# Optimization experiments

Measured on AMD Instinct MI355X. Metric: run time of the kernel, lower is better.

## Reference

```python
import jax, jax.numpy as jnp
import numpy as np

L = 3          # num_layer
E_DIM = 64     # emb_dim
B = 4          # graphs per batch
N = 20000      # nodes per graph
E = 320000     # edges per graph
IN_DIM = 21    # raw node feature dim (Linear(21, emb_dim))
BN_EPS = 1e-5


def setup_inputs() -> dict:
    key = jax.random.key(0)
    ks = jax.random.split(key, 16)
    h2 = 2 * E_DIM
    inp = {
        "x": jax.random.normal(ks[0], (B, N, IN_DIM), dtype=jnp.float32),
        "edge_index": jax.random.randint(ks[1], (B, 2, E), 0, N, dtype=jnp.int64),
        "edge_attr": jax.random.normal(ks[2], (B, E, 1), dtype=jnp.float32),
        # layer-0 input node embedding Linear(21, emb)
        "inW": jax.random.normal(ks[3], (IN_DIM, E_DIM), dtype=jnp.float32) * 0.1,
        "inb": jnp.zeros((E_DIM,), dtype=jnp.float32),
        # per-layer edge encoder Linear(1, emb)
        "edgeW": jax.random.normal(ks[4], (L, 1, E_DIM), dtype=jnp.float32) * 0.1,
        "edgeb": jnp.zeros((L, E_DIM), dtype=jnp.float32),
        # per-layer MLP: Linear(2e,2e) -> BN(2e) -> ReLU -> Linear(2e,e)
        "W1": jax.random.normal(ks[5], (L, h2, h2), dtype=jnp.float32) * 0.05,
        "b1": jnp.zeros((L, h2), dtype=jnp.float32),
        "gamma": jnp.ones((L, h2), dtype=jnp.float32),
        "beta": jnp.zeros((L, h2), dtype=jnp.float32),
        "W2": jax.random.normal(ks[6], (L, h2, E_DIM), dtype=jnp.float32) * 0.05,
        "b2": jnp.zeros((L, E_DIM), dtype=jnp.float32),
    }
    return inp


def _batchnorm_train(h, g, b):
    # BatchNorm1d in training mode: per-graph stats over the node dim, biased var
    m = h.mean(axis=0)
    v = jnp.mean((h - m) ** 2, axis=0)
    return (h - m) * jax.lax.rsqrt(v + BN_EPS) * g + b


def _gin_layer(xg, eig, eag, W1l, b1l, gl, bel, W2l, b2l):
    # xg [N,e], eig [2,E], eag [E,e]
    x_j = xg[eig[0]]                                   # gather source nodes [E,e]
    msg = jnp.concatenate([x_j, eag], axis=-1)         # [E,2e]
    aggr = jax.ops.segment_sum(msg, eig[1], num_segments=N)  # scatter-add [N,2e]
    h = aggr @ W1l + b1l
    h = _batchnorm_train(h, gl, bel)
    h = jax.nn.relu(h)
    return h @ W2l + b2l                               # [N,e]


def reference(x, edge_index, edge_attr, inW, inb, edgeW, edgeb, W1, b1, gamma, beta, W2, b2):
    h = x
    for l in range(L):
        ea = edge_attr @ edgeW[l] + edgeb[l]           # [B,E,e] edge embeddings
        if l == 0:
            h = h @ inW + inb                          # [B,N,e]
        h = jax.vmap(_gin_layer, in_axes=(0, 0, 0, None, None, None, None, None, None))(
            h, edge_index, ea, W1[l], b1[l], gamma[l], beta[l], W2[l], b2[l])
        if l < L - 1:                                  # drop_ratio=0 -> dropout is identity
            h = jax.nn.relu(h)
    return h  # JK='last'
```

## Files before the change

kernel.cpp:

```cpp
#include <hip/hip_runtime.h>
#include <hip/hip_bf16.h>

#define NB 4
#define NN 20000
#define NE 320000
#define IND 21
#define ED 64
#define H2 128
#define CAP 48
#define RNODES 2500
#define ECHUNK 2560
#define BN_EPS 1e-5f

typedef __attribute__((ext_vector_type(8))) short bf16x8;
typedef __attribute__((ext_vector_type(4))) float f32x4;

__device__ __forceinline__ short f2bf(float f) {
    unsigned u = __float_as_uint(f);
    u += 0x7fffu + ((u >> 16) & 1u);
    return (short)(u >> 16);
}


__global__ __launch_bounds__(256) void k_fill_direct(
    const int* __restrict__ ei, const float* __restrict__ eattr,
    int* __restrict__ cnt, unsigned int* __restrict__ bucket)
{
    const int b = blockIdx.y;
    const int range = blockIdx.x & 7;
    const int chunk = blockIdx.x >> 3;
    const int lo = range * RNODES, hi = lo + RNODES;
    const int* srcp = ei + (size_t)b * 2 * NE;
    const int* dstp = srcp + NE;
    const float* ap = eattr + (size_t)b * NE;
    #pragma unroll
    for (int it = 0; it < ECHUNK / 256; ++it) {
        const int e = chunk * ECHUNK + it * 256 + threadIdx.x;
        const int dst = dstp[e];
        if (dst >= lo && dst < hi) {
            const int src = srcp[e];
            const float a = ap[e];
            const int node = b * NN + dst;
            const int p = atomicAdd(&cnt[node], 1);
            if (p < CAP)
                bucket[(size_t)node * CAP + p] =
                    ((unsigned int)src & 0xffffu) | (__float_as_uint(a) & 0xffff0000u);
        }
    }
}

__global__ __launch_bounds__(256) void k_sattr(
    const unsigned int* __restrict__ bucket, const int* __restrict__ cnt,
    float* __restrict__ s_attr)
{
    const int n = blockIdx.x * 256 + threadIdx.x;
    if (n >= NB * NN) return;
    const int c = min(cnt[n], CAP);
    const unsigned int* row = bucket + (size_t)n * CAP;
    float s = 0.f;
    for (int j = 0; j < c; ++j)
        s += __uint_as_float(row[j] & 0xffff0000u);
    s_attr[n] = s;
}

__global__ __launch_bounds__(256) void k_in(
    const float* __restrict__ x, const float* __restrict__ inW,
    const float* __restrict__ inb, float* __restrict__ h)
{
    const int b = blockIdx.y;
    const int t = blockIdx.x * 256 + threadIdx.x;
    const int n = t >> 6;
    const int c = t & 63;
    if (n >= NN) return;
    const float* xr = x + ((size_t)b * NN + n) * IND;
    float acc = inb[c];
    #pragma unroll
    for (int k = 0; k < IND; ++k) acc += xr[k] * inW[k * ED + c];
    h[((size_t)b * NN + n) * ED + c] = acc;
}

__global__ __launch_bounds__(256) void k_wconv(
    const float* __restrict__ W1, const float* __restrict__ W2,
    short* __restrict__ W1T, short* __restrict__ W2T)
{
    const int lyr = blockIdx.x;
    for (int i = threadIdx.x; i < H2 * ED; i += 256) {
        const int j = i >> 6, k = i & 63;
        W1T[lyr * 8192 + i] = f2bf(W1[(size_t)lyr * H2 * H2 + k * H2 + j]);
    }
    for (int i = threadIdx.x; i < ED * H2; i += 256) {
        const int c = i >> 7, k = i & 127;
        W2T[lyr * 8192 + i] = f2bf(W2[(size_t)lyr * H2 * ED + k * ED + c]);
    }
}


__global__ void k_uv_zero(const float* __restrict__ edgeW, const float* __restrict__ edgeb,
                          const float* __restrict__ W1, float* __restrict__ uv,
                          float* __restrict__ stats, int l)
{
    const int j = threadIdx.x;
    ((float4*)stats)[j] = make_float4(0.f, 0.f, 0.f, 0.f);
    if (j >= H2) return;
    float u = 0.f, v = 0.f;
    for (int k = 0; k < ED; ++k) {
        const float w = W1[(size_t)l * H2 * H2 + (ED + k) * H2 + j];
        u += edgeW[l * ED + k] * w;
        v += edgeb[l * ED + k] * w;
    }
    uv[j] = u;
    uv[H2 + j] = v;
}

__global__ __launch_bounds__(256) void k_aggr_stats(
    const float* __restrict__ h, const unsigned int* __restrict__ bucket,
    const int* __restrict__ cnt_arr, const float* __restrict__ s_attr,
    const short* __restrict__ W1Tl, const float* __restrict__ b1l,
    const float* __restrict__ uv, short* __restrict__ aggr_bf,
    float* __restrict__ stats)
{
    __shared__ short w1t[H2 * 72];
    __shared__ short atb[16 * 72];
    __shared__ float sdl[16], ddl[16];
    __shared__ float uL[H2], vL[H2], bbL[H2];
    const int tid = threadIdx.x;
    const int g = blockIdx.x & 7;
    const int b = g >> 1;
    const int t = ((int)blockIdx.x >> 3) * 2 + (g & 1);
    const int n0 = t * 16;

    for (int i = tid; i < 1024; i += 256)
        *(uint4*)&w1t[(i >> 3) * 72 + (i & 7) * 8] = ((const uint4*)W1Tl)[i];
    if (tid < H2) { uL[tid] = uv[tid]; vL[tid] = uv[H2 + tid]; bbL[tid] = b1l[tid]; }

    {
        const int node = n0 + (tid >> 4);
        const int q = tid & 15;
        const int cnt = min(cnt_arr[b * NN + node], CAP);
        const unsigned int* row = bucket + (size_t)(b * NN + node) * CAP;
        const float* hb = h + (size_t)b * NN * ED + q * 4;
        float4 a0 = make_float4(0.f, 0.f, 0.f, 0.f);
        float4 a1 = make_float4(0.f, 0.f, 0.f, 0.f);
        int j = 0;
        for (; j + 4 <= cnt; j += 4) {
            const uint4 ss = *(const uint4*)(row + j);
            const float4 h0 = *(const float4*)&hb[(size_t)(ss.x & 0xffffu) * ED];
            const float4 h1 = *(const float4*)&hb[(size_t)(ss.y & 0xffffu) * ED];
            const float4 h2 = *(const float4*)&hb[(size_t)(ss.z & 0xffffu) * ED];
            const float4 h3 = *(const float4*)&hb[(size_t)(ss.w & 0xffffu) * ED];
            a0.x += h0.x + h1.x; a0.y += h0.y + h1.y; a0.z += h0.z + h1.z; a0.w += h0.w + h1.w;
            a1.x += h2.x + h3.x; a1.y += h2.y + h3.y; a1.z += h2.z + h3.z; a1.w += h2.w + h3.w;
        }
        for (; j < cnt; ++j) {
            const int s = row[j] & 0xffffu;
            const float4 hv = *(const float4*)&hb[(size_t)s * ED];
            a0.x += hv.x; a0.y += hv.y; a0.z += hv.z; a0.w += hv.w;
        }
        a0.x += a1.x; a0.y += a1.y; a0.z += a1.z; a0.w += a1.w;
        uint2 pk;
        pk.x = (unsigned short)f2bf(a0.x) | ((unsigned int)(unsigned short)f2bf(a0.y) << 16);
        pk.y = (unsigned short)f2bf(a0.z) | ((unsigned int)(unsigned short)f2bf(a0.w) << 16);
        *(uint2*)&atb[(tid >> 4) * 72 + q * 4] = pk;
        *(uint2*)&aggr_bf[((size_t)b * NN + node) * ED + q * 4] = pk;
    }
    if (tid < 16) sdl[tid] = s_attr[b * NN + n0 + tid];
    else if (tid < 32) ddl[tid - 16] = (float)cnt_arr[b * NN + n0 + tid - 16];
    __syncthreads();

    const int l = tid & 63;
    const int w = tid >> 6;
    const int m = l & 15, quad = l >> 4;
    f32x4 acc0 = {0.f, 0.f, 0.f, 0.f}, acc1 = {0.f, 0.f, 0.f, 0.f};
    #pragma unroll
    for (int kc = 0; kc < 2; ++kc) {
        const bf16x8 fa = *(const bf16x8*)&atb[m * 72 + kc * 32 + quad * 8];
        const bf16x8 fb0 = *(const bf16x8*)&w1t[((w * 2 + 0) * 16 + m) * 72 + kc * 32 + quad * 8];
        const bf16x8 fb1 = *(const bf16x8*)&w1t[((w * 2 + 1) * 16 + m) * 72 + kc * 32 + quad * 8];
        acc0 = __builtin_amdgcn_mfma_f32_16x16x32_bf16(fa, fb0, acc0, 0, 0, 0);
        acc1 = __builtin_amdgcn_mfma_f32_16x16x32_bf16(fa, fb1, acc1, 0, 0, 0);
    }
    float sa_r[4], dg_r[4];
    #pragma unroll
    for (int r = 0; r < 4; ++r) { sa_r[r] = sdl[quad * 4 + r]; dg_r[r] = ddl[quad * 4 + r]; }
    #pragma unroll
    for (int t2 = 0; t2 < 2; ++t2) {
        const int j = (w * 2 + t2) * 16 + m;
        const float u = uL[j], v = vL[j], bb = bbL[j];
        float ls = 0.f, lq = 0.f;
        #pragma unroll
        for (int r = 0; r < 4; ++r) {
            const float h1 = (t2 ? acc1[r] : acc0[r]) + sa_r[r] * u + dg_r[r] * v + bb;
            ls += h1; lq += h1 * h1;
        }
        ls += __shfl_xor(ls, 16); ls += __shfl_xor(ls, 32);
        lq += __shfl_xor(lq, 16); lq += __shfl_xor(lq, 32);
        if (l < 16) {
            atomicAdd(&stats[b * H2 + j], ls);
            atomicAdd(&stats[NB * H2 + b * H2 + j], lq);
        }
    }
}

__global__ void k_bn(const float* __restrict__ stats, const float* __restrict__ gamma,
                     const float* __restrict__ beta, float* __restrict__ scsh, int l)
{
    const int t = threadIdx.x;
    if (t >= NB * H2) return;
    const int j = t & 127;
    const float m = stats[t] * (1.f / NN);
    const float var = fmaxf(stats[NB * H2 + t] * (1.f / NN) - m * m, 0.f);
    const float rs = rsqrtf(var + BN_EPS);
    const float sc = gamma[l * H2 + j] * rs;
    scsh[t] = sc;
    scsh[NB * H2 + t] = beta[l * H2 + j] - m * sc;
}

__global__ __launch_bounds__(256) void k_mlp_out(
    const short* __restrict__ aggr_bf, const float* __restrict__ s_attr,
    const int* __restrict__ cnt_arr, const short* __restrict__ W1Tl,
    const short* __restrict__ W2Tl, const float* __restrict__ b1l,
    const float* __restrict__ uv, const float* __restrict__ scsh,
    const float* __restrict__ b2l, float* __restrict__ out, int relu_out)
{
    __shared__ short wt[H2 * 72];
    __shared__ short ab[32 * 72];
    __shared__ short pb[32 * 136];
    __shared__ float sdl[32], ddl[32];
    __shared__ float uL[H2], vL[H2], bbL[H2], scL[H2], shL[H2];
    const int tid = threadIdx.x;
    const int g = blockIdx.x & 7;
    const int b = g >> 1;
    const int t = ((int)blockIdx.x >> 3) * 2 + (g & 1);
    if (t >= NN / 32) return;
    const int n0 = t * 32;

    for (int i = tid; i < 1024; i += 256)
        *(uint4*)&wt[(i >> 3) * 72 + (i & 7) * 8] = ((const uint4*)W1Tl)[i];
    {
        const int i = tid;
        *(uint4*)&ab[(i >> 3) * 72 + (i & 7) * 8] =
            ((const uint4*)(aggr_bf + ((size_t)b * NN + n0) * ED))[i];
    }
    if (tid < 32) sdl[tid] = s_attr[b * NN + n0 + tid];
    else if (tid < 64) ddl[tid - 32] = (float)cnt_arr[b * NN + n0 + tid - 32];
    if (tid < H2) {
        uL[tid] = uv[tid]; vL[tid] = uv[H2 + tid]; bbL[tid] = b1l[tid];
        scL[tid] = scsh[b * H2 + tid]; shL[tid] = scsh[NB * H2 + b * H2 + tid];
    }
    __syncthreads();

    const int l = tid & 63;
    const int w = tid >> 6;
    const int m = l & 15, quad = l >> 4;
    const int mt = w & 1;
    {
        const int jb = (w >> 1) * 4;
        f32x4 acc[4];
        #pragma unroll
        for (int i = 0; i < 4; ++i) acc[i] = (f32x4){0.f, 0.f, 0.f, 0.f};
        #pragma unroll
        for (int kc = 0; kc < 2; ++kc) {
            const bf16x8 fa = *(const bf16x8*)&ab[(mt * 16 + m) * 72 + kc * 32 + quad * 8];
            #pragma unroll
            for (int t2 = 0; t2 < 4; ++t2) {
                const bf16x8 fb = *(const bf16x8*)&wt[((jb + t2) * 16 + m) * 72 + kc * 32 + quad * 8];
                acc[t2] = __builtin_amdgcn_mfma_f32_16x16x32_bf16(fa, fb, acc[t2], 0, 0, 0);
            }
        }
        float sa_r[4], dg_r[4];
        #pragma unroll
        for (int r = 0; r < 4; ++r) {
            const int row = mt * 16 + quad * 4 + r;
            sa_r[r] = sdl[row]; dg_r[r] = ddl[row];
        }
        #pragma unroll
        for (int t2 = 0; t2 < 4; ++t2) {
            const int j = (jb + t2) * 16 + m;
            const float u = uL[j], v = vL[j], bb = bbL[j];
            const float sc = scL[j], sh = shL[j];
            #pragma unroll
            for (int r = 0; r < 4; ++r) {
                const float h1 = acc[t2][r] + sa_r[r] * u + dg_r[r] * v + bb;
                pb[(mt * 16 + quad * 4 + r) * 136 + j] = f2bf(fmaxf(h1 * sc + sh, 0.f));
            }
        }
    }
    __syncthreads();
    for (int i = tid; i < 1024; i += 256)
        *(uint4*)&wt[(i >> 4) * 136 + (i & 15) * 8] = ((const uint4*)W2Tl)[i];
    __syncthreads();
    {
        const int nb = (w >> 1) * 2;
        f32x4 acc2[2];
        acc2[0] = (f32x4){0.f, 0.f, 0.f, 0.f};
        acc2[1] = (f32x4){0.f, 0.f, 0.f, 0.f};
        #pragma unroll
        for (int kc = 0; kc < 4; ++kc) {
            const bf16x8 fa = *(const bf16x8*)&pb[(mt * 16 + m) * 136 + kc * 32 + quad * 8];
            #pragma unroll
            for (int t2 = 0; t2 < 2; ++t2) {
                const bf16x8 fb = *(const bf16x8*)&wt[((nb + t2) * 16 + m) * 136 + kc * 32 + quad * 8];
                acc2[t2] = __builtin_amdgcn_mfma_f32_16x16x32_bf16(fa, fb, acc2[t2], 0, 0, 0);
            }
        }
        #pragma unroll
        for (int t2 = 0; t2 < 2; ++t2) {
            const int c = (nb + t2) * 16 + m;
            const float bb2 = b2l[c];
            #pragma unroll
            for (int r = 0; r < 4; ++r) {
                const int row = mt * 16 + quad * 4 + r;
                float o = acc2[t2][r] + bb2;
                if (relu_out) o = fmaxf(o, 0.f);
                out[((size_t)b * NN + n0 + row) * ED + c] = o;
            }
        }
    }
}


extern "C" void kernel_launch(void* const* d_in, const int* in_sizes, int n_in,
                              void* d_out, int out_size, void* d_ws, size_t ws_size,
                              hipStream_t stream) {
    const float* x     = (const float*)d_in[0];
    const int*   ei    = (const int*)d_in[1];
    const float* eattr = (const float*)d_in[2];
    const float* inW   = (const float*)d_in[3];
    const float* inb   = (const float*)d_in[4];
    const float* edgeW = (const float*)d_in[5];
    const float* edgeb = (const float*)d_in[6];
    const float* W1    = (const float*)d_in[7];
    const float* b1    = (const float*)d_in[8];
    const float* gamma = (const float*)d_in[9];
    const float* beta  = (const float*)d_in[10];
    const float* W2    = (const float*)d_in[11];
    const float* b2    = (const float*)d_in[12];
    float* h = (float*)d_out;

    float* s_attr = (float*)d_ws;
    int*   cnt    = (int*)(s_attr + NB * NN);
    unsigned int* bucket = (unsigned int*)(cnt + NB * NN);
    short* aggr_bf = (short*)(bucket + (size_t)NB * NN * CAP);
    short* W1T    = aggr_bf + (size_t)NB * NN * ED;
    short* W2T    = W1T + 3 * 8192;
    float* stats  = (float*)(W2T + 3 * 8192);
    float* scsh   = stats + 2 * NB * H2;
    float* uv     = scsh + 2 * NB * H2;

    hipMemsetAsync(cnt, 0, (size_t)NB * NN * sizeof(int), stream);

    const dim3 eg((NE / ECHUNK) * 8, NB);
    k_fill_direct<<<eg, 256, 0, stream>>>(ei, eattr, cnt, bucket);
    k_sattr<<<(NB * NN + 255) / 256, 256, 0, stream>>>(bucket, cnt, s_attr);
    k_in<<<dim3(NN * ED / 256, NB), 256, 0, stream>>>(x, inW, inb, h);
    k_wconv<<<3, 256, 0, stream>>>(W1, W2, W1T, W2T);

    const int nblk1 = NB * (NN / 16);
    const int nblk2 = ((NN / 32 + 1) / 2) * 16;
    for (int l = 0; l < 3; ++l) {
        k_uv_zero<<<1, 256, 0, stream>>>(edgeW, edgeb, W1, uv, stats, l);
        k_aggr_stats<<<nblk1, 256, 0, stream>>>(h, bucket, cnt, s_attr,
                                                W1T + l * 8192, b1 + l * H2, uv, aggr_bf, stats);
        k_bn<<<1, NB * H2, 0, stream>>>(stats, gamma, beta, scsh, l);
        k_mlp_out<<<nblk2, 256, 0, stream>>>(aggr_bf, s_attr, cnt,
                                             W1T + l * 8192, W2T + l * 8192, b1 + l * H2,
                                             uv, scsh, b2 + l * ED, h, (l < 2) ? 1 : 0);
    }
}
```

Baseline: 425.1 us.

## Store node features in fp16 and fold small prep kernels into main passes

New measurement: 386.1 us. -9.2%, faster.

```diff
diff --git a/kernel.cpp b/kernel.cpp
--- a/kernel.cpp
+++ b/kernel.cpp
@@ -1,5 +1,6 @@
 #include <hip/hip_runtime.h>
 #include <hip/hip_bf16.h>
+#include <hip/hip_fp16.h>
 
 #define NB 4
 #define NN 20000
@@ -49,23 +50,9 @@
     }
 }
 
-__global__ __launch_bounds__(256) void k_sattr(
-    const unsigned int* __restrict__ bucket, const int* __restrict__ cnt,
-    float* __restrict__ s_attr)
-{
-    const int n = blockIdx.x * 256 + threadIdx.x;
-    if (n >= NB * NN) return;
-    const int c = min(cnt[n], CAP);
-    const unsigned int* row = bucket + (size_t)n * CAP;
-    float s = 0.f;
-    for (int j = 0; j < c; ++j)
-        s += __uint_as_float(row[j] & 0xffff0000u);
-    s_attr[n] = s;
-}
-
 __global__ __launch_bounds__(256) void k_in(
     const float* __restrict__ x, const float* __restrict__ inW,
-    const float* __restrict__ inb, float* __restrict__ h)
+    const float* __restrict__ inb, __half* __restrict__ h)
 {
     const int b = blockIdx.y;
     const int t = blockIdx.x * 256 + threadIdx.x;
@@ -76,48 +63,45 @@
     float acc = inb[c];
     #pragma unroll
     for (int k = 0; k < IND; ++k) acc += xr[k] * inW[k * ED + c];
-    h[((size_t)b * NN + n) * ED + c] = acc;
-}
-
-__global__ __launch_bounds__(256) void k_wconv(
+    h[((size_t)b * NN + n) * ED + c] = __float2half(acc);
+}
+
+__global__ __launch_bounds__(256) void k_prep(
     const float* __restrict__ W1, const float* __restrict__ W2,
-    short* __restrict__ W1T, short* __restrict__ W2T)
-{
-    const int lyr = blockIdx.x;
-    for (int i = threadIdx.x; i < H2 * ED; i += 256) {
+    const float* __restrict__ edgeW, const float* __restrict__ edgeb,
+    short* __restrict__ W1T, short* __restrict__ W2T,
+    float* __restrict__ uv_all, float* __restrict__ stats_all)
+{
+    const int l = blockIdx.x;
+    const int tid = threadIdx.x;
+    ((float4*)(stats_all + l * 1024))[tid] = make_float4(0.f, 0.f, 0.f, 0.f);
+    for (int i = tid; i < H2 * ED; i += 256) {
         const int j = i >> 6, k = i & 63;
-        W1T[lyr * 8192 + i] = f2bf(W1[(size_t)lyr * H2 * H2 + k * H2 + j]);
-    }
-    for (int i = threadIdx.x; i < ED * H2; i += 256) {
+        W1T[l * 8192 + i] = f2bf(W1[(size_t)l * H2 * H2 + k * H2 + j]);
+    }
+    for (int i = tid; i < ED * H2; i += 256) {
         const int c = i >> 7, k = i & 127;
-        W2T[lyr * 8192 + i] = f2bf(W2[(size_t)lyr * H2 * ED + k * ED + c]);
-    }
-}
-
-
-__global__ void k_uv_zero(const float* __restrict__ edgeW, const float* __restrict__ edgeb,
-                          const float* __restrict__ W1, float* __restrict__ uv,
-                          float* __restrict__ stats, int l)
-{
-    const int j = threadIdx.x;
-    ((float4*)stats)[j] = make_float4(0.f, 0.f, 0.f, 0.f);
-    if (j >= H2) return;
-    float u = 0.f, v = 0.f;
-    for (int k = 0; k < ED; ++k) {
-        const float w = W1[(size_t)l * H2 * H2 + (ED + k) * H2 + j];
-        u += edgeW[l * ED + k] * w;
-        v += edgeb[l * ED + k] * w;
-    }
-    uv[j] = u;
-    uv[H2 + j] = v;
-}
+        W2T[l * 8192 + i] = f2bf(W2[(size_t)l * H2 * ED + k * ED + c]);
+    }
+    if (tid < H2) {
+        float u = 0.f, v = 0.f;
+        for (int k = 0; k < ED; ++k) {
+            const float w = W1[(size_t)l * H2 * H2 + (ED + k) * H2 + tid];
+            u += edgeW[l * ED + k] * w;
+            v += edgeb[l * ED + k] * w;
+        }
+        uv_all[l * 256 + tid] = u;
+        uv_all[l * 256 + H2 + tid] = v;
+    }
+}
+
 
 __global__ __launch_bounds__(256) void k_aggr_stats(
-    const float* __restrict__ h, const unsigned int* __restrict__ bucket,
-    const int* __restrict__ cnt_arr, const float* __restrict__ s_attr,
-    const short* __restrict__ W1Tl, const float* __restrict__ b1l,
-    const float* __restrict__ uv, short* __restrict__ aggr_bf,
-    float* __restrict__ stats)
+    const __half* __restrict__ h, const unsigned int* __restrict__ bucket,
+    const int* __restrict__ cnt_arr, const short* __restrict__ W1Tl,
+    const float* __restrict__ b1l, const float* __restrict__ uv_l,
+    short* __restrict__ aggr_bf, float* __restrict__ s_attr,
+    float* __restrict__ stats_l, int write_sattr)
 {
     __shared__ short w1t[H2 * 72];
     __shared__ short atb[16 * 72];
@@ -131,30 +115,47 @@
 
     for (int i = tid; i < 1024; i += 256)
         *(uint4*)&w1t[(i >> 3) * 72 + (i & 7) * 8] = ((const uint4*)W1Tl)[i];
-    if (tid < H2) { uL[tid] = uv[tid]; vL[tid] = uv[H2 + tid]; bbL[tid] = b1l[tid]; }
+    if (tid < H2) { uL[tid] = uv_l[tid]; vL[tid] = uv_l[H2 + tid]; bbL[tid] = b1l[tid]; }
 
     {
         const int node = n0 + (tid >> 4);
         const int q = tid & 15;
-        const int cnt = min(cnt_arr[b * NN + node], CAP);
+        const int cntraw = cnt_arr[b * NN + node];
+        const int cnt = min(cntraw, CAP);
         const unsigned int* row = bucket + (size_t)(b * NN + node) * CAP;
-        const float* hb = h + (size_t)b * NN * ED + q * 4;
+        const __half* hp = h + (size_t)b * NN * ED + q * 4;
         float4 a0 = make_float4(0.f, 0.f, 0.f, 0.f);
         float4 a1 = make_float4(0.f, 0.f, 0.f, 0.f);
+        float sa = 0.f;
         int j = 0;
         for (; j + 4 <= cnt; j += 4) {
             const uint4 ss = *(const uint4*)(row + j);
-            const float4 h0 = *(const float4*)&hb[(size_t)(ss.x & 0xffffu) * ED];
-            const float4 h1 = *(const float4*)&hb[(size_t)(ss.y & 0xffffu) * ED];
-            const float4 h2 = *(const float4*)&hb[(size_t)(ss.z & 0xffffu) * ED];
-            const float4 h3 = *(const float4*)&hb[(size_t)(ss.w & 0xffffu) * ED];
-            a0.x += h0.x + h1.x; a0.y += h0.y + h1.y; a0.z += h0.z + h1.z; a0.w += h0.w + h1.w;
-            a1.x += h2.x + h3.x; a1.y += h2.y + h3.y; a1.z += h2.z + h3.z; a1.w += h2.w + h3.w;
+            const uint2 r0 = *(const uint2*)(hp + (size_t)(ss.x & 0xffffu) * ED);
+            const uint2 r1 = *(const uint2*)(hp + (size_t)(ss.y & 0xffffu) * ED);
+            const uint2 r2 = *(const uint2*)(hp + (size_t)(ss.z & 0xffffu) * ED);
+            const uint2 r3 = *(const uint2*)(hp + (size_t)(ss.w & 0xffffu) * ED);
+            sa += __uint_as_float(ss.x & 0xffff0000u) + __uint_as_float(ss.y & 0xffff0000u)
+                + __uint_as_float(ss.z & 0xffff0000u) + __uint_as_float(ss.w & 0xffff0000u);
+            const float2 f0a = __half22float2(*(const __half2*)&r0.x);
+            const float2 f0b = __half22float2(*(const __half2*)&r0.y);
+            const float2 f1a = __half22float2(*(const __half2*)&r1.x);
+            const float2 f1b = __half22float2(*(const __half2*)&r1.y);
+            const float2 f2a = __half22float2(*(const __half2*)&r2.x);
+            const float2 f2b = __half22float2(*(const __half2*)&r2.y);
+            const float2 f3a = __half22float2(*(const __half2*)&r3.x);
+            const float2 f3b = __half22float2(*(const __half2*)&r3.y);
+            a0.x += f0a.x + f1a.x; a0.y += f0a.y + f1a.y;
+            a0.z += f0b.x + f1b.x; a0.w += f0b.y + f1b.y;
+            a1.x += f2a.x + f3a.x; a1.y += f2a.y + f3a.y;
+            a1.z += f2b.x + f3b.x; a1.w += f2b.y + f3b.y;
         }
         for (; j < cnt; ++j) {
-            const int s = row[j] & 0xffffu;
-            const float4 hv = *(const float4*)&hb[(size_t)s * ED];
-            a0.x += hv.x; a0.y += hv.y; a0.z += hv.z; a0.w += hv.w;
+            const unsigned e = row[j];
+            sa += __uint_as_float(e & 0xffff0000u);
+            const uint2 r0 = *(const uint2*)(hp + (size_t)(e & 0xffffu) * ED);
+            const float2 fa = __half22float2(*(const __half2*)&r0.x);
+            const float2 fb = __half22float2(*(const __half2*)&r0.y);
+            a0.x += fa.x; a0.y += fa.y; a0.z += fb.x; a0.w += fb.y;
         }
         a0.x += a1.x; a0.y += a1.y; a0.z += a1.z; a0.w += a1.w;
         uint2 pk;
@@ -162,9 +163,12 @@
         pk.y = (unsigned short)f2bf(a0.z) | ((unsigned int)(unsigned short)f2bf(a0.w) << 16);
         *(uint2*)&atb[(tid >> 4) * 72 + q * 4] = pk;
         *(uint2*)&aggr_bf[((size_t)b * NN + node) * ED + q * 4] = pk;
-    }
-    if (tid < 16) sdl[tid] = s_attr[b * NN + n0 + tid];
-    else if (tid < 32) ddl[tid - 16] = (float)cnt_arr[b * NN + n0 + tid - 16];
+        if (q == 0) {
+            sdl[tid >> 4] = sa;
+            ddl[tid >> 4] = (float)cntraw;
+            if (write_sattr) s_attr[b * NN + node] = sa;
+        }
+    }
     __syncthreads();
 
     const int l = tid & 63;
@@ -195,32 +199,20 @@
         ls += __shfl_xor(ls, 16); ls += __shfl_xor(ls, 32);
         lq += __shfl_xor(lq, 16); lq += __shfl_xor(lq, 32);
         if (l < 16) {
-            atomicAdd(&stats[b * H2 + j], ls);
-            atomicAdd(&stats[NB * H2 + b * H2 + j], lq);
-        }
-    }
-}
-
-__global__ void k_bn(const float* __restrict__ stats, const float* __restrict__ gamma,
-                     const float* __restrict__ beta, float* __restrict__ scsh, int l)
-{
-    const int t = threadIdx.x;
-    if (t >= NB * H2) return;
-    const int j = t & 127;
-    const float m = stats[t] * (1.f / NN);
-    const float var = fmaxf(stats[NB * H2 + t] * (1.f / NN) - m * m, 0.f);
-    const float rs = rsqrtf(var + BN_EPS);
-    const float sc = gamma[l * H2 + j] * rs;
-    scsh[t] = sc;
-    scsh[NB * H2 + t] = beta[l * H2 + j] - m * sc;
+            atomicAdd(&stats_l[b * H2 + j], ls);
+            atomicAdd(&stats_l[NB * H2 + b * H2 + j], lq);
+        }
+    }
 }
 
 __global__ __launch_bounds__(256) void k_mlp_out(
     const short* __restrict__ aggr_bf, const float* __restrict__ s_attr,
     const int* __restrict__ cnt_arr, const short* __restrict__ W1Tl,
     const short* __restrict__ W2Tl, const float* __restrict__ b1l,
-    const float* __restrict__ uv, const float* __restrict__ scsh,
-    const float* __restrict__ b2l, float* __restrict__ out, int relu_out)
+    const float* __restrict__ uv_l, const float* __restrict__ stats_l,
+    const float* __restrict__ gamma_l, const float* __restrict__ beta_l,
+    const float* __restrict__ b2l, __half* __restrict__ outh,
+    float* __restrict__ outf, int last)
 {
     __shared__ short wt[H2 * 72];
     __shared__ short ab[32 * 72];
@@ -236,16 +228,19 @@
 
     for (int i = tid; i < 1024; i += 256)
         *(uint4*)&wt[(i >> 3) * 72 + (i & 7) * 8] = ((const uint4*)W1Tl)[i];
-    {
-        const int i = tid;
-        *(uint4*)&ab[(i >> 3) * 72 + (i & 7) * 8] =
-            ((const uint4*)(aggr_bf + ((size_t)b * NN + n0) * ED))[i];
-    }
+    *(uint4*)&ab[(tid >> 3) * 72 + (tid & 7) * 8] =
+        ((const uint4*)(aggr_bf + ((size_t)b * NN + n0) * ED))[tid];
     if (tid < 32) sdl[tid] = s_attr[b * NN + n0 + tid];
     else if (tid < 64) ddl[tid - 32] = (float)cnt_arr[b * NN + n0 + tid - 32];
     if (tid < H2) {
-        uL[tid] = uv[tid]; vL[tid] = uv[H2 + tid]; bbL[tid] = b1l[tid];
-        scL[tid] = scsh[b * H2 + tid]; shL[tid] = scsh[NB * H2 + b * H2 + tid];
+        const int j = tid;
+        const float mm = stats_l[b * H2 + j] * (1.f / NN);
+        const float var = fmaxf(stats_l[NB * H2 + b * H2 + j] * (1.f / NN) - mm * mm, 0.f);
+        const float rs = rsqrtf(var + BN_EPS);
+        const float sc = gamma_l[j] * rs;
+        scL[j] = sc;
+        shL[j] = beta_l[j] - mm * sc;
+        uL[j] = uv_l[j]; vL[j] = uv_l[H2 + j]; bbL[j] = b1l[j];
     }
     __syncthreads();
 
@@ -310,9 +305,10 @@
             #pragma unroll
             for (int r = 0; r < 4; ++r) {
                 const int row = mt * 16 + quad * 4 + r;
+                const size_t idx = ((size_t)b * NN + n0 + row) * ED + c;
                 float o = acc2[t2][r] + bb2;
-                if (relu_out) o = fmaxf(o, 0.f);
-                out[((size_t)b * NN + n0 + row) * ED + c] = o;
+                if (last) outf[idx] = o;
+                else outh[idx] = __float2half(fmaxf(o, 0.f));
             }
         }
     }
@@ -335,35 +331,34 @@
     const float* beta  = (const float*)d_in[10];
     const float* W2    = (const float*)d_in[11];
     const float* b2    = (const float*)d_in[12];
-    float* h = (float*)d_out;
+    float* out = (float*)d_out;
 
     float* s_attr = (float*)d_ws;
     int*   cnt    = (int*)(s_attr + NB * NN);
     unsigned int* bucket = (unsigned int*)(cnt + NB * NN);
     short* aggr_bf = (short*)(bucket + (size_t)NB * NN * CAP);
-    short* W1T    = aggr_bf + (size_t)NB * NN * ED;
+    __half* hh    = (__half*)(aggr_bf + (size_t)NB * NN * ED);
+    short* W1T    = (short*)(hh + (size_t)NB * NN * ED);
     short* W2T    = W1T + 3 * 8192;
-    float* stats  = (float*)(W2T + 3 * 8192);
-    float* scsh   = stats + 2 * NB * H2;
-    float* uv     = scsh + 2 * NB * H2;
+    float* uv_all = (float*)(W2T + 3 * 8192);
+    float* stats  = uv_all + 3 * 256;
 
     hipMemsetAsync(cnt, 0, (size_t)NB * NN * sizeof(int), stream);
 
     const dim3 eg((NE / ECHUNK) * 8, NB);
     k_fill_direct<<<eg, 256, 0, stream>>>(ei, eattr, cnt, bucket);
-    k_sattr<<<(NB * NN + 255) / 256, 256, 0, stream>>>(bucket, cnt, s_attr);
-    k_in<<<dim3(NN * ED / 256, NB), 256, 0, stream>>>(x, inW, inb, h);
-    k_wconv<<<3, 256, 0, stream>>>(W1, W2, W1T, W2T);
+    k_in<<<dim3(NN * ED / 256, NB), 256, 0, stream>>>(x, inW, inb, hh);
+    k_prep<<<3, 256, 0, stream>>>(W1, W2, edgeW, edgeb, W1T, W2T, uv_all, stats);
 
     const int nblk1 = NB * (NN / 16);
     const int nblk2 = ((NN / 32 + 1) / 2) * 16;
     for (int l = 0; l < 3; ++l) {
-        k_uv_zero<<<1, 256, 0, stream>>>(edgeW, edgeb, W1, uv, stats, l);
-        k_aggr_stats<<<nblk1, 256, 0, stream>>>(h, bucket, cnt, s_attr,
-                                                W1T + l * 8192, b1 + l * H2, uv, aggr_bf, stats);
-        k_bn<<<1, NB * H2, 0, stream>>>(stats, gamma, beta, scsh, l);
+        k_aggr_stats<<<nblk1, 256, 0, stream>>>(hh, bucket, cnt,
+            W1T + l * 8192, b1 + l * H2, uv_all + l * 256,
+            aggr_bf, s_attr, stats + l * 1024, (l == 0) ? 1 : 0);
         k_mlp_out<<<nblk2, 256, 0, stream>>>(aggr_bf, s_attr, cnt,
-                                             W1T + l * 8192, W2T + l * 8192, b1 + l * H2,
-                                             uv, scsh, b2 + l * ED, h, (l < 2) ? 1 : 0);
-    }
-}
+            W1T + l * 8192, W2T + l * 8192, b1 + l * H2, uv_all + l * 256,
+            stats + l * 1024, gamma + l * H2, beta + l * H2, b2 + l * ED,
+            hh, out, (l == 2) ? 1 : 0);
+    }
+}
```
